# Kernel optimization log

Measured on AMD Instinct MI355X. Metric: run time of the kernel, lower is better.

The kernel has to match this reference:

```python
import jax, jax.numpy as jnp
import numpy as np

L, H, D, HS = 6, 8, 512, 64
EPS = 1e-5


def _ln(x, g, b):
    m = jnp.mean(x, -1, keepdims=True)
    v = jnp.mean((x - m) ** 2, -1, keepdims=True)
    return (x - m) * jax.lax.rsqrt(v + EPS) * g + b


def _posenc(T, C):
    pos = jnp.arange(T, dtype=jnp.float32)[:, None]
    div = jnp.exp(jnp.arange(0, C, 2, dtype=jnp.float32) * (-jnp.log(10000.0) / C))
    pe = jnp.zeros((T, C), jnp.float32)
    pe = pe.at[:, 0::2].set(jnp.sin(pos * div))
    pe = pe.at[:, 1::2].set(jnp.cos(pos * div))
    return pe


def setup_inputs() -> dict:
    B, T, F, V, E, O = 8, 1024, 32, 7, 16, 49
    key = jax.random.key(0)
    ks = jax.random.split(key, 16)
    s = 0.02
    inp = {
        'code': jax.random.randint(ks[0], (B, T, F), 0, V),
        'lengths': jax.random.randint(ks[1], (B,), T // 2, T + 1),
        'emb': s * jax.random.normal(ks[2], (V, E), jnp.float32),
        'Wq': s * jax.random.normal(ks[3], (L, H, D, HS), jnp.float32),
        'Wk': s * jax.random.normal(ks[4], (L, H, D, HS), jnp.float32),
        'Wv': s * jax.random.normal(ks[5], (L, H, D, HS), jnp.float32),
        'Wo': s * jax.random.normal(ks[6], (L, D, D), jnp.float32),
        'bo': jnp.zeros((L, D), jnp.float32),
        'W1': s * jax.random.normal(ks[7], (L, D, 4 * D), jnp.float32),
        'b1': jnp.zeros((L, 4 * D), jnp.float32),
        'W2': s * jax.random.normal(ks[8], (L, 4 * D, D), jnp.float32),
        'b2': jnp.zeros((L, D), jnp.float32),
        'ln1_g': jnp.ones((L, D), jnp.float32),
        'ln1_b': jnp.zeros((L, D), jnp.float32),
        'ln2_g': jnp.ones((L, D), jnp.float32),
        'ln2_b': jnp.zeros((L, D), jnp.float32),
        'lnf_g': jnp.ones((D,), jnp.float32),
        'lnf_b': jnp.zeros((D,), jnp.float32),
        'attn_w': s * jax.random.normal(ks[9], (D, 1), jnp.float32),
        'attn_b': jnp.zeros((1,), jnp.float32),
        'head_w': s * jax.random.normal(ks[10], (D, 49), jnp.float32),
        'head_b': jnp.zeros((49,), jnp.float32),
    }
    return inp


def reference(code, lengths, emb, Wq, Wk, Wv, Wo, bo, W1, b1, W2, b2,
              ln1_g, ln1_b, ln2_g, ln2_b, lnf_g, lnf_b,
              attn_w, attn_b, head_w, head_b):
    B, T, F = code.shape
    # token embedding (B,T,F,E) -> (B,T,D) plus sinusoidal positions
    x = emb[code].reshape(B, T, D) + _posenc(T, D)
    mask = jnp.arange(T) < lengths[:, None]          # (B,T) valid positions
    col_mask = mask[:, None, None, :]                # mask key columns
    row_mask = mask[:, None, :, None]                # zero padded query rows
    for l in range(L):
        xn = _ln(x, ln1_g[l], ln1_b[l])
        q = jnp.einsum('btd,hde->bhte', xn, Wq[l])
        k = jnp.einsum('btd,hde->bhte', xn, Wk[l])
        v = jnp.einsum('btd,hde->bhte', xn, Wv[l])
        wei = jnp.einsum('bhte,bhse->bhts', q, k) * (HS ** -0.5)
        wei = jnp.where(col_mask, wei, -jnp.inf)
        wei = jax.nn.softmax(wei, axis=-1)
        wei = jnp.where(row_mask, wei, 0.0)
        o = jnp.einsum('bhts,bhse->bthe', wei, v).reshape(B, T, H * HS)
        x = x + o @ Wo[l] + bo[l]
        xn = _ln(x, ln2_g[l], ln2_b[l])
        x = x + jax.nn.gelu(xn @ W1[l] + b1[l], approximate=False) @ W2[l] + b2[l]
    x = _ln(x, lnf_g, lnf_b)
    # attention pooling over time
    scores = x @ attn_w + attn_b                     # (B,T,1)
    scores = jnp.where(mask[:, :, None], scores, -jnp.inf)
    aw = jax.nn.softmax(scores, axis=1)
    summary = jnp.sum(aw * x, axis=1)                # (B,D)
    logits = summary @ head_w + head_b               # (B,49)
    return logits
```

## Files before the change

kernel.cpp:

```cpp
#include <hip/hip_runtime.h>
#include <math.h>

#define TT 1024
#define BB 8
#define DD 512
#define HH 8
#define HSZ 64
#define LL 6
#define FF4 2048

typedef __attribute__((ext_vector_type(8))) short short8;
typedef __attribute__((ext_vector_type(4))) float floatx4;
typedef unsigned short ushort_t;
typedef unsigned int uint_t;

__device__ __forceinline__ ushort_t f2bf(float f) {
  uint_t u = __float_as_uint(f);
  u += 0x7fff + ((u >> 16) & 1);
  return (ushort_t)(u >> 16);
}
__device__ __forceinline__ float bf2f(ushort_t h) {
  return __uint_as_float(((uint_t)h) << 16);
}


__global__ __launch_bounds__(256) void k_embed(const int* __restrict__ code,
                                               const float* __restrict__ emb,
                                               float* __restrict__ x,
                                               const int* __restrict__ lengths) {
  int idx = blockIdx.x * 256 + threadIdx.x;
  int c = idx & (DD - 1);
  int bt = idx >> 9;
  int t = bt & (TT - 1);
  if (t >= lengths[bt >> 10]) return;
  int f = c >> 4, e = c & 15;
  int vv = code[bt * 32 + f];
  int i = c >> 1;
  float freq = expf((float)(2 * i) * (-9.210340371976184f / 512.f));
  float ang = (float)t * freq;
  float pe = (c & 1) ? cosf(ang) : sinf(ang);
  x[idx] = emb[vv * 16 + e] + pe;
}

__global__ __launch_bounds__(256) void k_ln(const float* __restrict__ x,
                                            ushort_t* __restrict__ yB,
                                            float* __restrict__ yF,
                                            const float* __restrict__ g,
                                            const float* __restrict__ b,
                                            const float* __restrict__ aw,
                                            const float* __restrict__ ab,
                                            float* __restrict__ scores,
                                            const int* __restrict__ lengths) {
  int row0 = blockIdx.x * 4;
  if ((row0 & (TT - 1)) >= lengths[row0 >> 10]) return;
  int wave = threadIdx.x >> 6, lane = threadIdx.x & 63;
  int row = row0 + wave;
  const float* xr = x + (size_t)row * DD;
  float v[8];
  *(float4*)&v[0] = *(const float4*)(xr + lane * 8);
  *(float4*)&v[4] = *(const float4*)(xr + lane * 8 + 4);
  float s = 0.f;
#pragma unroll
  for (int j = 0; j < 8; ++j) s += v[j];
#pragma unroll
  for (int off = 32; off; off >>= 1) s += __shfl_down(s, off, 64);
  float mean = __shfl(s, 0, 64) * (1.f / DD);
  float qv = 0.f;
#pragma unroll
  for (int j = 0; j < 8; ++j) { float d = v[j] - mean; qv += d * d; }
#pragma unroll
  for (int off = 32; off; off >>= 1) qv += __shfl_down(qv, off, 64);
  float rs = rsqrtf(__shfl(qv, 0, 64) * (1.f / DD) + 1e-5f);
  float ov[8];
  float sdot = 0.f;
#pragma unroll
  for (int e = 0; e < 8; ++e) {
    int c = lane * 8 + e;
    ov[e] = (v[e] - mean) * rs * g[c] + b[c];
    if (scores) sdot += ov[e] * aw[c];
  }
  if (yB) {
    short8 o8;
#pragma unroll
    for (int e = 0; e < 8; ++e) o8[e] = (short)f2bf(ov[e]);
    size_t ad = (((size_t)(row >> 4) * 16 + (lane >> 2)) << 9) + ((lane & 3) * 16 + (row & 15)) * 8;
    *(short8*)(yB + ad) = o8;
  } else {
    float* yr = yF + (size_t)row * DD + lane * 8;
    *(float4*)yr = *(float4*)&ov[0];
    *(float4*)(yr + 4) = *(float4*)&ov[4];
  }
  if (scores) {
#pragma unroll
    for (int off = 32; off; off >>= 1) sdot += __shfl_down(sdot, off, 64);
    if (lane == 0) scores[row] = sdot + ab[0];
  }
}

__global__ __launch_bounds__(256) void k_packw(const float* __restrict__ in,
                                               ushort_t* __restrict__ out,
                                               int Nin, long in_ms, int nh,
                                               long os_l, int nblk, int Kout) {
  __shared__ float t4[64][65];
  int mz = blockIdx.z;
  const float* ip = in + (size_t)mz * in_ms;
  ushort_t* op = out + (size_t)(mz / nh) * os_l;
  int nbase = (mz % nh) * nblk + blockIdx.y * 64;
  int k0 = blockIdx.x * 64;
  int cc = threadIdx.x & 63, r0 = threadIdx.x >> 6;
#pragma unroll
  for (int i = 0; i < 16; ++i) {
    int r = r0 * 16 + i;
    t4[r][cc] = ip[(size_t)(k0 + r) * Nin + (nbase - (mz % nh) * nblk) + cc];
  }
  __syncthreads();
#pragma unroll
  for (int half = 0; half < 2; ++half) {
    int c = threadIdx.x + half * 256;
    int joct = c >> 6, nl = c & 63;
    int n = nbase + nl, k = k0 + joct * 8;
    short8 v8;
#pragma unroll
    for (int e = 0; e < 8; ++e) v8[e] = (short)f2bf(t4[joct * 8 + e][nl]);
    size_t ad = (((size_t)(n >> 4) * (Kout >> 5) + (k >> 5)) << 9) + (((k >> 3) & 3) * 16 + (n & 15)) * 8;
    *(short8*)(op + ad) = v8;
  }
}

template <int BN>
__global__ __launch_bounds__(256, 3) void k_sgemm(const ushort_t* __restrict__ Apk,
                                                  const ushort_t* __restrict__ Bpk,
                                                  const float* __restrict__ resid,
                                                  const float* __restrict__ bias,
                                                  float* __restrict__ outF,
                                                  ushort_t* __restrict__ outB,
                                                  int M, int N, int K, int mode,
                                                  const int* __restrict__ lengths) {
  constexpr int MT = (BN == 128) ? 4 : 2;
  constexpr int NT = 4;
  constexpr int NA = 8;
  constexpr int NB = BN / 16;
  constexpr int NFRAG = NA + NB;
  constexpr int NF = NFRAG / 4;
  constexpr int BUFU = NFRAG * 512;
  __shared__ ushort_t lds[(BN == 128) ? 20480 : 2 * BUFU];

  const int tid = threadIdx.x;
  const int w = tid >> 6, lane = tid & 63;
  const int quad = lane >> 4, l16 = lane & 15;
  const int gx = N / BN;
  int id = blockIdx.x;
  int bx = (id >> 3) % gx;
  int by = (id / (8 * gx)) * 8 + (id & 7);
  const int row0 = by * 128, col0 = bx * BN;
  if (lengths && (row0 & (TT - 1)) >= lengths[row0 >> 10]) return;
  const int nk = K >> 5;

  const int wrow0 = (BN == 128) ? row0 + (w >> 1) * 64 : row0 + w * 32;
  const int wcol0 = (BN == 128) ? col0 + (w & 1) * 64 : col0;
  const int ar16 = (wrow0 - row0) >> 4;
  const int bc16 = NA + ((wcol0 - col0) >> 4);

  const ushort_t* gbase[NF];
#pragma unroll
  for (int i = 0; i < NF; ++i) {
    int f = w * NF + i;
    if (f < NA)
      gbase[i] = Apk + (((size_t)((row0 >> 4) + f) * nk) << 9) + lane * 8;
    else
      gbase[i] = Bpk + (((size_t)((col0 >> 4) + (f - NA)) * nk) << 9) + lane * 8;
  }
  const int ldst = (w * NF) * 512 + lane * 8;

  floatx4 acc[MT][NT] = {};
  short8 greg[NF];

#pragma unroll
  for (int i = 0; i < NF; ++i) greg[i] = *(const short8*)(gbase[i]);
#pragma unroll
  for (int i = 0; i < NF; ++i) *(short8*)&lds[ldst + i * 512] = greg[i];
  __syncthreads();

  int bufo = 0;
  for (int kc = 0; kc + 1 < nk; ++kc) {
#pragma unroll
    for (int i = 0; i < NF; ++i)
      greg[i] = *(const short8*)(gbase[i] + ((size_t)(kc + 1) << 9));
    short8 af[MT], bfv[NT];
#pragma unroll
    for (int mt = 0; mt < MT; ++mt) af[mt] = *(const short8*)&lds[bufo + (ar16 + mt) * 512 + lane * 8];
#pragma unroll
    for (int nt = 0; nt < NT; ++nt) bfv[nt] = *(const short8*)&lds[bufo + (bc16 + nt) * 512 + lane * 8];
#pragma unroll
    for (int mt = 0; mt < MT; ++mt)
#pragma unroll
      for (int nt = 0; nt < NT; ++nt)
        acc[mt][nt] = __builtin_amdgcn_mfma_f32_16x16x32_bf16(af[mt], bfv[nt], acc[mt][nt], 0, 0, 0);
    const int nbufo = bufo ^ BUFU;
#pragma unroll
    for (int i = 0; i < NF; ++i) *(short8*)&lds[nbufo + ldst + i * 512] = greg[i];
    __syncthreads();
    bufo = nbufo;
  }
  {
    short8 af[MT], bfv[NT];
#pragma unroll
    for (int mt = 0; mt < MT; ++mt) af[mt] = *(const short8*)&lds[bufo + (ar16 + mt) * 512 + lane * 8];
#pragma unroll
    for (int nt = 0; nt < NT; ++nt) bfv[nt] = *(const short8*)&lds[bufo + (bc16 + nt) * 512 + lane * 8];
#pragma unroll
    for (int mt = 0; mt < MT; ++mt)
#pragma unroll
      for (int nt = 0; nt < NT; ++nt)
        acc[mt][nt] = __builtin_amdgcn_mfma_f32_16x16x32_bf16(af[mt], bfv[nt], acc[mt][nt], 0, 0, 0);
  }

  if (BN == 128 && mode == 2) {
    __syncthreads();
    ushort_t* Cb = &lds[w * 5120];
#pragma unroll
    for (int mt = 0; mt < MT; ++mt)
#pragma unroll
      for (int nt = 0; nt < NT; ++nt) {
        floatx4 a4 = acc[mt][nt];
#pragma unroll
        for (int r = 0; r < 4; ++r) {
          float val = a4[r] + bias[wcol0 + nt * 16 + l16];
          val = 0.5f * val * (1.f + erff(val * 0.7071067811865475f));
          Cb[(mt * 16 + quad * 4 + r) * 80 + nt * 16 + l16] = f2bf(val);
        }
      }
#pragma unroll
    for (int mt2 = 0; mt2 < 4; ++mt2)
#pragma unroll
      for (int kt2 = 0; kt2 < 2; ++kt2) {
        short8 v8 = *(const short8*)&Cb[(mt2 * 16 + l16) * 80 + kt2 * 32 + quad * 8];
        size_t ad = ((((size_t)(wrow0 >> 4) + mt2) * (N >> 5) + (wcol0 >> 5) + kt2) << 9) + lane * 8;
        *(short8*)(outB + ad) = v8;
      }
  } else {
    const float qscale = (mode == 3 && col0 < 512) ? 0.125f : 1.0f;
#pragma unroll
    for (int mt = 0; mt < MT; ++mt)
#pragma unroll
      for (int nt = 0; nt < NT; ++nt) {
        floatx4 a4 = acc[mt][nt];
#pragma unroll
        for (int r = 0; r < 4; ++r) {
          int row = wrow0 + mt * 16 + quad * 4 + r;
          int col = wcol0 + nt * 16 + l16;
          float val = a4[r];
          if (bias) val += bias[col];
          size_t idx = (size_t)row * N + col;
          if (mode == 1) outF[idx] = val + resid[idx];
          else outB[idx] = f2bf(val * qscale);
        }
      }
  }
}

__global__ __launch_bounds__(256) void k_attn(const ushort_t* __restrict__ qkv,
                                              const int* __restrict__ lengths,
                                              ushort_t* __restrict__ o) {
  __shared__ ushort_t Ks[64 * 72];
  __shared__ ushort_t Vt[64 * 72];
  __shared__ ushort_t Ps[4][16 * 72];
  const int tid = threadIdx.x;
  const int w = tid >> 6, lane = tid & 63;
  const int quad = lane >> 4, l16 = lane & 15;
  const int tile = blockIdx.x & 15;
  const int bh = blockIdx.x >> 4;
  const int b = bh >> 3, h = bh & 7;
  const int len = lengths[b];
  if (tile * 64 >= len) return;
  const int tqa = tile * 64 + w * 16 + l16;
  const ushort_t* qp = qkv + ((size_t)(b * TT + tqa)) * 1536 + h * HSZ + quad * 8;
  short8 qf0 = *(const short8*)qp;
  short8 qf1 = *(const short8*)(qp + 32);
  floatx4 oacc[4] = {};
  float lsum[4] = {0.f, 0.f, 0.f, 0.f};
  const int skey = tid >> 2, sseg = (tid & 3) << 4;
  const int vkp = (tid & 31) << 1, vds = (tid >> 5) << 3;
  const int nkt = (len + 63) >> 6;
  for (int kt = 0; kt < nkt; ++kt) {
    const int s0 = kt * 64;
    __syncthreads();
    {
      const ushort_t* kp = qkv + ((size_t)(b * TT + s0 + skey)) * 1536 + 512 + h * HSZ + sseg;
      short8 k0 = *(const short8*)kp;
      short8 k1 = *(const short8*)(kp + 8);
      *(short8*)&Ks[skey * 72 + sseg] = k0;
      *(short8*)&Ks[skey * 72 + sseg + 8] = k1;
      const ushort_t* vp0 = qkv + ((size_t)(b * TT + s0 + vkp)) * 1536 + 1024 + h * HSZ + vds;
      short8 v0 = *(const short8*)vp0;
      short8 v1 = *(const short8*)(vp0 + 1536);
#pragma unroll
      for (int i = 0; i < 8; ++i) {
        ushort2 pr;
        pr.x = (ushort_t)v0[i];
        pr.y = (ushort_t)v1[i];
        *(ushort2*)&Vt[(vds + i) * 72 + vkp] = pr;
      }
    }
    __syncthreads();
    floatx4 sacc[4] = {};
#pragma unroll
    for (int nt = 0; nt < 4; ++nt) {
      short8 kf0 = *(const short8*)&Ks[(nt * 16 + l16) * 72 + quad * 8];
      short8 kf1 = *(const short8*)&Ks[(nt * 16 + l16) * 72 + 32 + quad * 8];
      sacc[nt] = __builtin_amdgcn_mfma_f32_16x16x32_bf16(qf0, kf0, sacc[nt], 0, 0, 0);
      sacc[nt] = __builtin_amdgcn_mfma_f32_16x16x32_bf16(qf1, kf1, sacc[nt], 0, 0, 0);
    }
    float p[4][4];
    if (kt == nkt - 1) {
#pragma unroll
      for (int nt = 0; nt < 4; ++nt) {
        bool valid = (s0 + nt * 16 + l16 < len);
#pragma unroll
        for (int r = 0; r < 4; ++r) p[nt][r] = valid ? __expf(sacc[nt][r]) : 0.f;
      }
    } else {
#pragma unroll
      for (int nt = 0; nt < 4; ++nt)
#pragma unroll
        for (int r = 0; r < 4; ++r) p[nt][r] = __expf(sacc[nt][r]);
    }
#pragma unroll
    for (int r = 0; r < 4; ++r)
#pragma unroll
      for (int nt = 0; nt < 4; ++nt) {
        lsum[r] += p[nt][r];
        Ps[w][(quad * 4 + r) * 72 + nt * 16 + l16] = f2bf(p[nt][r]);
      }
    short8 pf0 = *(const short8*)&Ps[w][l16 * 72 + quad * 8];
    short8 pf1 = *(const short8*)&Ps[w][l16 * 72 + 32 + quad * 8];
#pragma unroll
    for (int nt = 0; nt < 4; ++nt) {
      short8 vf0 = *(const short8*)&Vt[(nt * 16 + l16) * 72 + quad * 8];
      short8 vf1 = *(const short8*)&Vt[(nt * 16 + l16) * 72 + 32 + quad * 8];
      oacc[nt] = __builtin_amdgcn_mfma_f32_16x16x32_bf16(pf0, vf0, oacc[nt], 0, 0, 0);
      oacc[nt] = __builtin_amdgcn_mfma_f32_16x16x32_bf16(pf1, vf1, oacc[nt], 0, 0, 0);
    }
  }
#pragma unroll
  for (int off = 1; off < 16; off <<= 1) {
#pragma unroll
    for (int r = 0; r < 4; ++r) lsum[r] += __shfl_xor(lsum[r], off, 64);
  }
#pragma unroll
  for (int r = 0; r < 4; ++r) {
    int t = tile * 64 + w * 16 + quad * 4 + r;
    float inv = (t < len) ? 1.f / lsum[r] : 0.f;
#pragma unroll
    for (int nt = 0; nt < 4; ++nt)
      Ps[w][(quad * 4 + r) * 72 + nt * 16 + l16] = f2bf(oacc[nt][r] * inv);
  }
  const int mtile = b * 64 + tile * 4 + w;
#pragma unroll
  for (int kt2 = 0; kt2 < 2; ++kt2) {
    short8 v8 = *(const short8*)&Ps[w][l16 * 72 + kt2 * 32 + quad * 8];
    size_t ad = (((size_t)mtile * 16 + h * 2 + kt2) << 9) + lane * 8;
    *(short8*)(o + ad) = v8;
  }
}

__global__ __launch_bounds__(256) void k_softw(const float* __restrict__ scores,
                                               const int* __restrict__ lengths,
                                               float* __restrict__ wts) {
  __shared__ float red[8];
  int tid = threadIdx.x, b = blockIdx.x;
  int len = lengths[b];
  const float* sb = scores + b * TT;
  float m = -1e30f;
  for (int t = tid; t < len; t += 256) m = fmaxf(m, sb[t]);
#pragma unroll
  for (int off = 32; off; off >>= 1) m = fmaxf(m, __shfl_down(m, off, 64));
  if ((tid & 63) == 0) red[tid >> 6] = m;
  __syncthreads();
  m = fmaxf(fmaxf(red[0], red[1]), fmaxf(red[2], red[3]));
  float ssum = 0.f;
  for (int t = tid; t < len; t += 256) ssum += __expf(sb[t] - m);
#pragma unroll
  for (int off = 32; off; off >>= 1) ssum += __shfl_down(ssum, off, 64);
  if ((tid & 63) == 0) red[4 + (tid >> 6)] = ssum;
  __syncthreads();
  float inv = 1.f / (red[4] + red[5] + red[6] + red[7]);
  for (int t = tid; t < TT; t += 256)
    wts[b * TT + t] = (t < len) ? __expf(sb[t] - m) * inv : 0.f;
}

__global__ __launch_bounds__(256) void k_wsum(const float* __restrict__ xf,
                                              const float* __restrict__ wts,
                                              float* __restrict__ partial,
                                              const int* __restrict__ lengths) {
  int b = blockIdx.x, c = blockIdx.y, tid = threadIdx.x;
  float* pp = partial + ((size_t)b * 16 + c) * DD;
  if (c * 64 >= lengths[b]) {
    pp[tid] = 0.f;
    pp[tid + 256] = 0.f;
    return;
  }
  const float* xb = xf + ((size_t)b * TT + c * 64) * DD;
  const float* wb = wts + b * TT + c * 64;
  float a0 = 0.f, a1 = 0.f;
  for (int t = 0; t < 64; ++t) {
    float wv = wb[t];
    a0 += wv * xb[(size_t)t * DD + tid];
    a1 += wv * xb[(size_t)t * DD + tid + 256];
  }
  pp[tid] = a0;
  pp[tid + 256] = a1;
}

__global__ __launch_bounds__(64) void k_head(const float* __restrict__ partial,
                                             const float* __restrict__ head_w,
                                             const float* __restrict__ head_b,
                                             float* __restrict__ out) {
  __shared__ float ssum[DD];
  int b = blockIdx.x, tid = threadIdx.x;
  for (int d = tid; d < DD; d += 64) {
    float s = 0.f;
#pragma unroll
    for (int c = 0; c < 16; ++c) s += partial[((size_t)b * 16 + c) * DD + d];
    ssum[d] = s;
  }
  __syncthreads();
  if (tid < 49) {
    float s = head_b[tid];
    for (int d = 0; d < DD; ++d) s += ssum[d] * head_w[d * 49 + tid];
    out[b * 49 + tid] = s;
  }
}

extern "C" void kernel_launch(void* const* d_in, const int* in_sizes, int n_in,
                              void* d_out, int out_size, void* d_ws, size_t ws_size,
                              hipStream_t stream) {
  const int* code = (const int*)d_in[0];
  const int* lengths = (const int*)d_in[1];
  const float* emb = (const float*)d_in[2];
  const float* Wq = (const float*)d_in[3];
  const float* Wk = (const float*)d_in[4];
  const float* Wv = (const float*)d_in[5];
  const float* Wo = (const float*)d_in[6];
  const float* bo = (const float*)d_in[7];
  const float* W1 = (const float*)d_in[8];
  const float* b1 = (const float*)d_in[9];
  const float* W2 = (const float*)d_in[10];
  const float* b2 = (const float*)d_in[11];
  const float* ln1_g = (const float*)d_in[12];
  const float* ln1_b = (const float*)d_in[13];
  const float* ln2_g = (const float*)d_in[14];
  const float* ln2_b = (const float*)d_in[15];
  const float* lnf_g = (const float*)d_in[16];
  const float* lnf_b = (const float*)d_in[17];
  const float* attn_w = (const float*)d_in[18];
  const float* attn_b = (const float*)d_in[19];
  const float* head_w = (const float*)d_in[20];
  const float* head_b = (const float*)d_in[21];
  float* out = (float*)d_out;

  const size_t NTOK = (size_t)BB * TT;
  float* x = (float*)d_ws;
  ushort_t* xn = (ushort_t*)(x + NTOK * DD);
  ushort_t* un = xn + NTOK * DD;
  ushort_t* qkv = un;
  ushort_t* h1 = un;
  float* xf = (float*)un;
  ushort_t* wqpk = un + (size_t)NTOK * FF4;
  ushort_t* wopk = wqpk + (size_t)LL * 1536 * 512;
  ushort_t* w1pk = wopk + (size_t)LL * 512 * 512;
  ushort_t* w2pk = w1pk + (size_t)LL * 512 * FF4;
  float* scores = (float*)(w2pk + (size_t)LL * FF4 * 512);
  float* wts = scores + NTOK;
  float* partial = wts + NTOK;

  k_packw<<<dim3(8, 1, 48), 256, 0, stream>>>(Wq, wqpk,              64, (long)512 * 64, 8, (long)1536 * 512, 64, 512);
  k_packw<<<dim3(8, 1, 48), 256, 0, stream>>>(Wk, wqpk + 512 * 512,  64, (long)512 * 64, 8, (long)1536 * 512, 64, 512);
  k_packw<<<dim3(8, 1, 48), 256, 0, stream>>>(Wv, wqpk + 1024 * 512, 64, (long)512 * 64, 8, (long)1536 * 512, 64, 512);
  k_packw<<<dim3(8, 8, 6), 256, 0, stream>>>(Wo, wopk, 512, (long)512 * 512, 1, (long)512 * 512, 0, 512);
  k_packw<<<dim3(8, 32, 6), 256, 0, stream>>>(W1, w1pk, 2048, (long)512 * 2048, 1, (long)2048 * 512, 0, 512);
  k_packw<<<dim3(32, 8, 6), 256, 0, stream>>>(W2, w2pk, 512, (long)2048 * 512, 1, (long)512 * 2048, 0, 2048);

  k_embed<<<dim3((unsigned)((NTOK * DD) / 256)), dim3(256), 0, stream>>>(code, emb, x, lengths);

  for (int l = 0; l < LL; ++l) {
    k_ln<<<dim3(NTOK / 4), 256, 0, stream>>>(x, xn, nullptr, ln1_g + l * DD, ln1_b + l * DD,
                                             nullptr, nullptr, nullptr, lengths);
    k_sgemm<128><<<dim3(768), 256, 0, stream>>>(xn, wqpk + (size_t)l * 1536 * 512, nullptr, nullptr,
                                                nullptr, qkv, (int)NTOK, 1536, 512, 3, lengths);
    k_attn<<<dim3(BB * HH * (TT / 64)), 256, 0, stream>>>(qkv, lengths, xn);
    k_sgemm<64><<<dim3(512), 256, 0, stream>>>(xn, wopk + (size_t)l * 512 * 512, x, bo + l * DD,
                                               x, nullptr, (int)NTOK, 512, 512, 1, lengths);
    k_ln<<<dim3(NTOK / 4), 256, 0, stream>>>(x, xn, nullptr, ln2_g + l * DD, ln2_b + l * DD,
                                             nullptr, nullptr, nullptr, lengths);
    k_sgemm<128><<<dim3(1024), 256, 0, stream>>>(xn, w1pk + (size_t)l * 512 * FF4, nullptr, b1 + l * FF4,
                                                 nullptr, h1, (int)NTOK, FF4, 512, 2, lengths);
    k_sgemm<64><<<dim3(512), 256, 0, stream>>>(h1, w2pk + (size_t)l * FF4 * 512, x, b2 + l * DD,
                                               x, nullptr, (int)NTOK, 512, 2048, 1, lengths);
  }
  k_ln<<<dim3(NTOK / 4), 256, 0, stream>>>(x, nullptr, xf, lnf_g, lnf_b,
                                           attn_w, attn_b, scores, lengths);
  k_softw<<<dim3(BB), 256, 0, stream>>>(scores, lengths, wts);
  k_wsum<<<dim3(BB, 16), 256, 0, stream>>>(xf, wts, partial, lengths);
  k_head<<<dim3(BB), 64, 0, stream>>>(partial, head_w, head_b, out);
}
```

Baseline: 1.394 ms.

## Stage GEMM tiles with direct global-to-LDS loads and use 64x64 tiles for N=512 GEMMs

The GEMM kernel now loads its operand fragments straight from global memory into LDS with global_load_lds. Before, it staged them through registers and wrote them out after the MFMA block. The narrow output GEMMs (Wo and W2) switch from 128x64 tiles to 64x64 tiles with a 2x2 warp layout and twice as many blocks, for better CU occupancy and a higher occupancy hint. The direct LDS path frees registers and store instructions. It depends on correct ordering between the asynchronous LDS writes and the barrier, and smaller tiles reduce data reuse per block.

```diff
diff --git a/kernel.cpp b/kernel.cpp
--- a/kernel.cpp
+++ b/kernel.cpp
@@ -21,6 +21,12 @@
 }
 __device__ __forceinline__ float bf2f(ushort_t h) {
   return __uint_as_float(((uint_t)h) << 16);
+}
+
+typedef const __attribute__((address_space(1))) uint_t* gas_t;
+typedef __attribute__((address_space(3))) uint_t* las_t;
+__device__ __forceinline__ void stage16(const ushort_t* g, ushort_t* l) {
+  __builtin_amdgcn_global_load_lds((gas_t)g, (las_t)l, 16, 0, 0);
 }
 
 
@@ -127,23 +133,23 @@
   }
 }
 
-template <int BN>
-__global__ __launch_bounds__(256, 3) void k_sgemm(const ushort_t* __restrict__ Apk,
-                                                  const ushort_t* __restrict__ Bpk,
-                                                  const float* __restrict__ resid,
-                                                  const float* __restrict__ bias,
-                                                  float* __restrict__ outF,
-                                                  ushort_t* __restrict__ outB,
-                                                  int M, int N, int K, int mode,
-                                                  const int* __restrict__ lengths) {
-  constexpr int MT = (BN == 128) ? 4 : 2;
-  constexpr int NT = 4;
-  constexpr int NA = 8;
+template <int BM, int BN>
+__global__ __launch_bounds__(256, (BM == 128) ? 3 : 4) void k_agemm(const ushort_t* __restrict__ Apk,
+                                                                    const ushort_t* __restrict__ Bpk,
+                                                                    const float* __restrict__ resid,
+                                                                    const float* __restrict__ bias,
+                                                                    float* __restrict__ outF,
+                                                                    ushort_t* __restrict__ outB,
+                                                                    int M, int N, int K, int mode,
+                                                                    const int* __restrict__ lengths) {
+  constexpr int MT = BM / 32;
+  constexpr int NT = BN / 32;
+  constexpr int NA = BM / 16;
   constexpr int NB = BN / 16;
   constexpr int NFRAG = NA + NB;
   constexpr int NF = NFRAG / 4;
   constexpr int BUFU = NFRAG * 512;
-  __shared__ ushort_t lds[(BN == 128) ? 20480 : 2 * BUFU];
+  __shared__ ushort_t lds[(BM == 128) ? 20480 : 2 * NFRAG * 512];
 
   const int tid = threadIdx.x;
   const int w = tid >> 6, lane = tid & 63;
@@ -152,40 +158,39 @@
   int id = blockIdx.x;
   int bx = (id >> 3) % gx;
   int by = (id / (8 * gx)) * 8 + (id & 7);
-  const int row0 = by * 128, col0 = bx * BN;
+  const int row0 = by * BM, col0 = bx * BN;
   if (lengths && (row0 & (TT - 1)) >= lengths[row0 >> 10]) return;
   const int nk = K >> 5;
 
-  const int wrow0 = (BN == 128) ? row0 + (w >> 1) * 64 : row0 + w * 32;
-  const int wcol0 = (BN == 128) ? col0 + (w & 1) * 64 : col0;
-  const int ar16 = (wrow0 - row0) >> 4;
-  const int bc16 = NA + ((wcol0 - col0) >> 4);
-
-  const ushort_t* gbase[NF];
+  const int wrow0 = row0 + (w >> 1) * (BM / 2);
+  const int wcol0 = col0 + (w & 1) * (BN / 2);
+  const int ar16 = (w >> 1) * MT;
+  const int bc16 = NA + (w & 1) * NT;
+
+  const ushort_t* gsrc[NF];
+  int slot[NF];
 #pragma unroll
   for (int i = 0; i < NF; ++i) {
     int f = w * NF + i;
     if (f < NA)
-      gbase[i] = Apk + (((size_t)((row0 >> 4) + f) * nk) << 9) + lane * 8;
+      gsrc[i] = Apk + (((size_t)((row0 >> 4) + f) * nk) << 9) + lane * 8;
     else
-      gbase[i] = Bpk + (((size_t)((col0 >> 4) + (f - NA)) * nk) << 9) + lane * 8;
-  }
-  const int ldst = (w * NF) * 512 + lane * 8;
+      gsrc[i] = Bpk + (((size_t)((col0 >> 4) + (f - NA)) * nk) << 9) + lane * 8;
+    slot[i] = f * 512;
+  }
 
   floatx4 acc[MT][NT] = {};
-  short8 greg[NF];
-
-#pragma unroll
-  for (int i = 0; i < NF; ++i) greg[i] = *(const short8*)(gbase[i]);
-#pragma unroll
-  for (int i = 0; i < NF; ++i) *(short8*)&lds[ldst + i * 512] = greg[i];
+
+#pragma unroll
+  for (int i = 0; i < NF; ++i) stage16(gsrc[i], &lds[slot[i]]);
   __syncthreads();
 
   int bufo = 0;
   for (int kc = 0; kc + 1 < nk; ++kc) {
+    const int nbufo = bufo ^ BUFU;
 #pragma unroll
     for (int i = 0; i < NF; ++i)
-      greg[i] = *(const short8*)(gbase[i] + ((size_t)(kc + 1) << 9));
+      stage16(gsrc[i] + ((size_t)(kc + 1) << 9), &lds[nbufo + slot[i]]);
     short8 af[MT], bfv[NT];
 #pragma unroll
     for (int mt = 0; mt < MT; ++mt) af[mt] = *(const short8*)&lds[bufo + (ar16 + mt) * 512 + lane * 8];
@@ -196,9 +201,6 @@
 #pragma unroll
       for (int nt = 0; nt < NT; ++nt)
         acc[mt][nt] = __builtin_amdgcn_mfma_f32_16x16x32_bf16(af[mt], bfv[nt], acc[mt][nt], 0, 0, 0);
-    const int nbufo = bufo ^ BUFU;
-#pragma unroll
-    for (int i = 0; i < NF; ++i) *(short8*)&lds[nbufo + ldst + i * 512] = greg[i];
     __syncthreads();
     bufo = nbufo;
   }
@@ -215,7 +217,7 @@
         acc[mt][nt] = __builtin_amdgcn_mfma_f32_16x16x32_bf16(af[mt], bfv[nt], acc[mt][nt], 0, 0, 0);
   }
 
-  if (BN == 128 && mode == 2) {
+  if (BM == 128 && mode == 2) {
     __syncthreads();
     ushort_t* Cb = &lds[w * 5120];
 #pragma unroll
@@ -486,17 +488,17 @@
   for (int l = 0; l < LL; ++l) {
     k_ln<<<dim3(NTOK / 4), 256, 0, stream>>>(x, xn, nullptr, ln1_g + l * DD, ln1_b + l * DD,
                                              nullptr, nullptr, nullptr, lengths);
-    k_sgemm<128><<<dim3(768), 256, 0, stream>>>(xn, wqpk + (size_t)l * 1536 * 512, nullptr, nullptr,
-                                                nullptr, qkv, (int)NTOK, 1536, 512, 3, lengths);
+    k_agemm<128, 128><<<dim3(768), 256, 0, stream>>>(xn, wqpk + (size_t)l * 1536 * 512, nullptr, nullptr,
+                                                     nullptr, qkv, (int)NTOK, 1536, 512, 3, lengths);
     k_attn<<<dim3(BB * HH * (TT / 64)), 256, 0, stream>>>(qkv, lengths, xn);
-    k_sgemm<64><<<dim3(512), 256, 0, stream>>>(xn, wopk + (size_t)l * 512 * 512, x, bo + l * DD,
-                                               x, nullptr, (int)NTOK, 512, 512, 1, lengths);
+    k_agemm<64, 64><<<dim3(1024), 256, 0, stream>>>(xn, wopk + (size_t)l * 512 * 512, x, bo + l * DD,
+                                                    x, nullptr, (int)NTOK, 512, 512, 1, lengths);
     k_ln<<<dim3(NTOK / 4), 256, 0, stream>>>(x, xn, nullptr, ln2_g + l * DD, ln2_b + l * DD,
                                              nullptr, nullptr, nullptr, lengths);
-    k_sgemm<128><<<dim3(1024), 256, 0, stream>>>(xn, w1pk + (size_t)l * 512 * FF4, nullptr, b1 + l * FF4,
-                                                 nullptr, h1, (int)NTOK, FF4, 512, 2, lengths);
-    k_sgemm<64><<<dim3(512), 256, 0, stream>>>(h1, w2pk + (size_t)l * FF4 * 512, x, b2 + l * DD,
-                                               x, nullptr, (int)NTOK, 512, 2048, 1, lengths);
+    k_agemm<128, 128><<<dim3(1024), 256, 0, stream>>>(xn, w1pk + (size_t)l * 512 * FF4, nullptr, b1 + l * FF4,
+                                                      nullptr, h1, (int)NTOK, FF4, 512, 2, lengths);
+    k_agemm<64, 64><<<dim3(1024), 256, 0, stream>>>(h1, w2pk + (size_t)l * FF4 * 512, x, b2 + l * DD,
+                                                    x, nullptr, (int)NTOK, 512, 2048, 1, lengths);
   }
   k_ln<<<dim3(NTOK / 4), 256, 0, stream>>>(x, nullptr, xf, lnf_g, lnf_b,
                                            attn_w, attn_b, scores, lengths);
```

Result: faster. 1.236 ms (-11.3%).
